# Kernel tuning notes

Hardware: AMD Instinct MI355X
Metric: run time of the kernel (lower is better)

Reference implementation:

```python
import jax, jax.numpy as jnp
import numpy as np

PS = 7        # pooled_size == conved_size
IMG = 300     # img_size
FMAP = 19     # feature map spatial size
SMAX = IMG // 16  # clamp max (18), matches torch long clamp(0, 300/16)
EPS = 1e-5


def _bn(x, g, b, m, v):
    scale = (g * jax.lax.rsqrt(v + EPS))[None, :, None, None]
    return x * scale + (b - m * g * jax.lax.rsqrt(v + EPS))[None, :, None, None]


def _conv(x, W, b=None, pad=1):
    y = jax.lax.conv_general_dilated(x, W, (1, 1), [(pad, pad), (pad, pad)],
                                     dimension_numbers=('NCHW', 'OIHW', 'NCHW'))
    if b is not None:
        y = y + b[None, :, None, None]
    return y


def _adaptive_w(lo, hi):
    # Per-ROI adaptive-avg-pool weights over the full 19-wide axis.
    # lo, hi: [B,R] inclusive crop bounds. Returns [B,R,PS,FMAP].
    H = hi - lo + 1                                  # crop length per ROI
    i = jnp.arange(PS)
    s = (i[None, None, :] * H[..., None]) // PS      # bin start (floor)
    e = -((-(i[None, None, :] + 1) * H[..., None]) // PS)  # bin end (ceil)
    rows = jnp.arange(FMAP)
    start = lo[..., None, None] + s[..., None]
    stop = lo[..., None, None] + e[..., None]
    mask = (rows >= start) & (rows < stop)
    denom = jnp.maximum(e - s, 1).astype(jnp.float32)[..., None]
    return mask.astype(jnp.float32) / denom


def setup_inputs() -> dict:
    key = jax.random.key(0)
    ks = jax.random.split(key, 6)
    B, R = 8, 128
    return {
        'roi_proposal': jax.random.uniform(ks[0], (B, 1, R, 5), dtype=jnp.float32),
        'features': jax.random.normal(ks[1], (B, 1024, FMAP, FMAP), dtype=jnp.float32),
        'W1': jax.random.normal(ks[2], (256, 1024, 3, 3), dtype=jnp.float32) * 0.02,
        'b1': jnp.zeros((256,), jnp.float32),
        'g1': jnp.ones((256,), jnp.float32),
        'be1': jnp.zeros((256,), jnp.float32),
        'm1': jnp.zeros((256,), jnp.float32),
        'v1': jnp.ones((256,), jnp.float32),
        'W2': jax.random.normal(ks[3], (256, 256, 3, 3), jnp.float32) * 0.05,
        'b2': jnp.zeros((256,), jnp.float32),
        'g2': jnp.ones((256,), jnp.float32),
        'be2': jnp.zeros((256,), jnp.float32),
        'm2': jnp.zeros((256,), jnp.float32),
        'v2': jnp.ones((256,), jnp.float32),
        'W3': jax.random.normal(ks[4], (32, 256, 1, 1), jnp.float32) * 0.1,
        'g3': jnp.ones((32,), jnp.float32),
        'be3': jnp.zeros((32,), jnp.float32),
        'm3': jnp.zeros((32,), jnp.float32),
        'v3': jnp.ones((32,), jnp.float32),
    }


def reference(roi_proposal, features, W1, b1, g1, be1, m1, v1,
              W2, b2, g2, be2, m2, v2, W3, g3, be3, m3, v3):
    # rois[..., 1:] * img_size / 16, then trunc to long (coords are >= 0)
    rl = (roi_proposal[:, 0, :, 1:] * (IMG / 16.0)).astype(jnp.int32)  # [B,R,4]
    c = jnp.clip(rl, 0, SMAX)
    xmin, ymin, xmax, ymax = c[..., 0], c[..., 1], c[..., 2], c[..., 3]
    valid = (xmax > xmin) & (ymax > ymin)                              # [B,R]
    B, R = valid.shape

    # fused crop + adaptive avg pool as two small pooling matmuls per ROI
    Wy = _adaptive_w(ymin, ymax)   # [B,R,7,19]
    Wx = _adaptive_w(xmin, xmax)   # [B,R,7,19]
    pooled = jnp.einsum('brph,bchw,brqw->brcpq', Wy, features, Wx)     # [B,R,1024,7,7]

    x = pooled.reshape(B * R, 1024, PS, PS)
    x = jax.nn.relu(_bn(_conv(x, W1, b1), g1, be1, m1, v1))
    x = jax.nn.relu(_bn(_conv(x, W2, b2), g2, be2, m2, v2))
    x = jax.nn.relu(_bn(_conv(x, W3, None, pad=0), g3, be3, m3, v3))
    out = x.reshape(B, R, 32, PS, PS) * valid[:, :, None, None, None]

    # compact valid ROIs to the front per batch (stable), invalid slots zeroed
    perm = jnp.argsort((~valid).astype(jnp.int32), axis=1, stable=True)
    out_c = jax.vmap(lambda o, p: o[p])(out, perm)                     # [B,R,32,7,7]
    er = rl.astype(jnp.float32) * (16.0 / IMG) * valid[..., None]
    er_c = jax.vmap(lambda o, p: o[p])(er, perm)[:, None]              # [B,1,R,4]
    keep_count = valid.sum(axis=1).astype(jnp.int32)                   # [B]
    return er_c, out_c, keep_count
```

## Files before the change

kernel.cpp:

```cpp
#include <hip/hip_runtime.h>
#include <cstddef>
#include <cstdint>

typedef unsigned short u16;
typedef unsigned int u32;
typedef __attribute__((ext_vector_type(8))) short short8;
typedef __attribute__((ext_vector_type(4))) float f32x4;

#define NB 8
#define NR 128
#define NPOS 49
#define EPSV 1e-5f
#define NSLOT 512

#define OUT_OC   4096
#define OUT_KEEP 1609728

static constexpr size_t OFF_META = 256;
static constexpr size_t OFF_KEEP = 33024;
static constexpr size_t OFF_W1Q  = 40960;
static constexpr size_t OFF_W2Q  = OFF_W1Q + 4718592;
static constexpr size_t OFF_W3   = OFF_W2Q + 1179648;
static constexpr size_t OFF_X1S  = OFF_W3  + 32768;
static constexpr size_t OFF_AP   = OFF_X1S + 13107200;
static constexpr size_t WS_NEED  = OFF_AP  + 51380224;

static __device__ __forceinline__ u16 f2bf(float f) {
  union { float f; u32 u; } x; x.f = f;
  u32 r = 0x7fffu + ((x.u >> 16) & 1u);
  return (u16)((x.u + r) >> 16);
}

__device__ __forceinline__ void int_body(const float* __restrict__ feat, float* __restrict__ S,
                                         int b, int cg, float* F)
{
  int tid = threadIdx.x;
  const float* fb = feat + ((size_t)b * 1024 + cg * 64) * 361;
#pragma unroll 1
  for (int i = tid; i < 64 * 361; i += 256) F[i] = fb[i];
  __syncthreads();
  if (tid < 64) {
    int ch = tid;
    const float* fp = F + ch * 361;
    float* Sp = S + (size_t)b * 400 * 1024 + cg * 64 + ch;
    float prev[20];
#pragma unroll
    for (int w = 0; w < 20; ++w) { prev[w] = 0.f; Sp[(size_t)w * 1024] = 0.f; }
    for (int h = 0; h < 19; ++h) {
      float run = 0.f;
      float* Sr = Sp + (size_t)(h + 1) * 20 * 1024;
      Sr[0] = 0.f;
#pragma unroll
      for (int w = 0; w < 19; ++w) {
        run += fp[h * 19 + w];
        float v = run + prev[w + 1];
        Sr[(size_t)(w + 1) * 1024] = v;
        prev[w + 1] = v;
      }
    }
  }
}

__device__ __forceinline__ void packw_body(const float* __restrict__ W, u16* __restrict__ wq,
                                           int IC, int c, int og, float* F)
{
  int tid = threadIdx.x, oc0 = og * 32;
#pragma unroll 1
  for (int i = tid; i < 18432; i += 256) {
    int ocr = i / 576, r = i - ocr * 576;
    F[i] = W[(size_t)(oc0 + ocr) * IC * 9 + c * 576 + r];
  }
  __syncthreads();
#pragma unroll 1
  for (int w = tid; w < 18432; w += 256) {
    int j = w & 7, lane = (w >> 3) & 63, rest = w >> 9;
    int ntr = rest & 1, kk = rest >> 1;
    int k9i = kk >> 1, ks = kk & 1;
    int ocr = ntr * 16 + (lane & 15);
    int icr = ks * 32 + ((lane >> 4) & 3) * 8 + j;
    int bid_ = (c * 9 + k9i) * 2 + ks;
    wq[((size_t)bid_ * 1024 + (oc0 / 16 + ntr) * 64 + lane) * 8 + j] = f2bf(F[ocr * 576 + icr * 9 + k9i]);
  }
}

__global__ __launch_bounds__(256) void k_prep(
    const float* __restrict__ feat, float* __restrict__ S,
    const float* __restrict__ W1, const float* __restrict__ W2, const float* __restrict__ W3,
    u16* __restrict__ w1q, u16* __restrict__ w2q, u16* __restrict__ w3q,
    const float* __restrict__ roi, int* __restrict__ cnt,
    int* __restrict__ meta, int* __restrict__ keepd, float* __restrict__ out)
{
  __shared__ float SH[23104];
  int bx = blockIdx.x;
  if (bx < 128) { int_body(feat, S, bx >> 4, bx & 15, SH); return; }
  if (bx < 256) { packw_body(W1, w1q, 1024, (bx - 128) >> 3, (bx - 128) & 7, SH); return; }
  if (bx < 288) { packw_body(W2, w2q, 256, (bx - 256) >> 3, (bx - 256) & 7, SH); return; }
  if (bx == 288) {
    for (int i = threadIdx.x; i < 8192; i += 256) {
      int oc = i >> 8, ic = i & 255;
      int kk = ic >> 5;
      int lane = ((ic >> 3) & 3) * 16 + (oc & 15);
      int nt16 = oc >> 4;
      int j = ic & 7;
      w3q[((size_t)((kk * 2 + nt16) * 64) + lane) * 8 + j] = f2bf(W3[i]);
    }
    return;
  }
  int b = bx - 289, t = threadIdx.x;
  int* sval = (int*)SH;
  int* spre = sval + 128;
  int rl[4], cl[4], valid = 0;
  if (t < 128) {
    const float* rp = roi + (size_t)(b * NR + t) * 5;
#pragma unroll
    for (int j = 0; j < 4; ++j) {
      rl[j] = (int)(rp[1 + j] * 18.75f);
      cl[j] = min(max(rl[j], 0), 18);
    }
    valid = (cl[2] > cl[0]) && (cl[3] > cl[1]) ? 1 : 0;
    sval[t] = valid;
  }
  __syncthreads();
  if (t == 0) {
    int s = 0;
    for (int i = 0; i < 128; ++i) { spre[i] = s; s += sval[i]; }
    spre[128] = s;
    keepd[b] = s;
    out[OUT_KEEP + b] = (float)s;
  }
  __syncthreads();
  if (t < 128) {
    int keep = spre[128];
    if (valid) {
      int dst = spre[t];
      int slot = atomicAdd(cnt, 1);
      int* mt = meta + slot * 8;
      mt[0] = b; mt[1] = dst;
      mt[2] = cl[1]; mt[3] = cl[3];
      mt[4] = cl[0]; mt[5] = cl[2];
#pragma unroll
      for (int j = 0; j < 4; ++j)
        out[(size_t)(b * NR + dst) * 4 + j] = (float)rl[j] * (16.0f / 300.0f);
    }
    if (t >= keep) {
#pragma unroll
      for (int j = 0; j < 4; ++j) out[(size_t)(b * NR + t) * 4 + j] = 0.f;
    }
  }
}

__global__ __launch_bounds__(256) void k_pool(
    const int* __restrict__ cnt, const int* __restrict__ meta,
    const float* __restrict__ S, u16* __restrict__ Apool)
{
  int cv = *cnt; if (cv > NSLOT) cv = NSLOT;
  int slot = blockIdx.x;
  if (slot >= cv) return;
  const int* mt_ = meta + slot * 8;
  int b = mt_[0], ylo = mt_[2], yhi = mt_[3], xlo = mt_[4], xhi = mt_[5];
  int Hy = yhi - ylo + 1, Hx = xhi - xlo + 1;
  const float* Sb = S + (size_t)b * 400 * 1024;
  u16* Ap = Apool + (size_t)slot * 50176;
  int base = blockIdx.y * 25088, end = base + 25088;
  int tid = threadIdx.x;
#pragma unroll 1
  for (int t0 = base + tid; t0 < end; t0 += 1024) {
#pragma unroll
    for (int u = 0; u < 4; ++u) {
      int t = t0 + u * 256;
      if (t < end) {
        int ch = t & 63, r = t >> 6;
        int bin = r % 49, c = r / 49;
        int p = bin / 7, q = bin - 7 * p;
        int sy = (p * Hy) / 7, ey = ((p + 1) * Hy + 6) / 7;
        int sx = (q * Hx) / 7, ex = ((q + 1) * Hx + 6) / 7;
        int y0 = ylo + sy, y1 = ylo + ey, x0 = xlo + sx, x1 = xlo + ex;
        const float* Sc = Sb + c * 64 + ch;
        float v = Sc[(size_t)(y1 * 20 + x1) * 1024] - Sc[(size_t)(y0 * 20 + x1) * 1024]
                - Sc[(size_t)(y1 * 20 + x0) * 1024] + Sc[(size_t)(y0 * 20 + x0) * 1024];
        v /= (float)((ey - sy) * (ex - sx));
        Ap[(size_t)c * 3136 + bin * 64 + ch] = f2bf(v);
      }
    }
  }
}

template<int STR>
__device__ __forceinline__ void build_aoffp(int n, int kq, int (&aoffp)[9][2]) {
#pragma unroll
  for (int t9 = 0; t9 < 9; ++t9) {
    int off[4];
#pragma unroll
    for (int mt = 0; mt < 4; ++mt) {
      int lm = mt * 16 + n;
      int mv = lm < 49;
      int lm2 = mv ? lm : 0;
      int p = lm2 / 7, q = lm2 - 7 * p;
      int ky = t9 / 3, kx = t9 - 3 * (t9 / 3);
      int ry = p + ky - 1, rx = q + kx - 1;
      int ok = mv && ry >= 0 && ry < 7 && rx >= 0 && rx < 7;
      int rr = ok ? ry * 7 + rx : 49;
      off[mt] = rr * STR + kq * 8;
    }
    aoffp[t9][0] = (off[0] & 0xFFFF) | (off[1] << 16);
    aoffp[t9][1] = (off[2] & 0xFFFF) | (off[3] << 16);
  }
}

__global__ __launch_bounds__(512) void k_conv1(
    const int* __restrict__ cnt, const u16* __restrict__ Apool, const u16* __restrict__ wq,
    const float* __restrict__ bb, const float* __restrict__ gg, const float* __restrict__ bec,
    const float* __restrict__ mm, const float* __restrict__ vv,
    u16* __restrict__ x1)
{
  int cv = *cnt; if (cv > NSLOT) cv = NSLOT;
  int slot0 = blockIdx.x * 4, ocq = blockIdx.y;
  if (slot0 >= cv) return;

  __shared__ __align__(16) u16 panels[16 * 3600];
  float* red = (float*)panels;

  int tid = threadIdx.x, lane = tid & 63, wave = tid >> 6;
  int kh = wave >> 2, roi4 = wave & 3;
  int n = lane & 15, kq = lane >> 4;

  for (int i = tid; i < 16 * 36; i += 512) {
    int sp = i / 36, w2 = i - sp * 36;
    ((u32*)(panels + sp * 3600 + 49 * 72))[w2] = 0;
  }

  int aoffp[9][2];
  build_aoffp<72>(n, kq, aoffp);
  f32x4 acc[4][4];
#pragma unroll
  for (int i = 0; i < 4; ++i)
#pragma unroll
    for (int j = 0; j < 4; ++j) acc[i][j] = (f32x4){0.f, 0.f, 0.f, 0.f};

  const u16* pf = wq + (size_t)(ocq * 4) * 512 + (size_t)lane * 8 + (size_t)(kh * 8) * 18 * 8192;
  short8 bbuf[2][4];
#pragma unroll
  for (int nt = 0; nt < 4; ++nt) bbuf[0][nt] = *(const short8*)(pf + nt * 512);
#pragma unroll
  for (int nt = 0; nt < 4; ++nt) bbuf[1][nt] = *(const short8*)(pf + 8192 + nt * 512);
  pf += (size_t)2 * 8192;

  uint4 sbuf[7];
  auto load_issue = [&](int ca, int cb) {
#pragma unroll
    for (int j = 0; j < 7; ++j) {
      int t = tid + j * 512;
      if (t < 3136) {
        int khs = t >= 1568 ? 1 : 0;
        int e2 = t - khs * 1568;
        int rr = e2 / 392, e = e2 - rr * 392;
        int c = khs ? cb : ca;
        int sl = slot0 + rr; if (sl >= cv) sl = cv - 1;
        sbuf[j] = *((const uint4*)(Apool + ((size_t)sl * 16 + c) * 3136) + e);
      }
    }
  };
  auto write_sbuf = [&](int B) {
#pragma unroll
    for (int j = 0; j < 7; ++j) {
      int t = tid + j * 512;
      if (t < 3136) {
        int khs = t >= 1568 ? 1 : 0;
        int e2 = t - khs * 1568;
        int rr = e2 / 392, e = e2 - rr * 392;
        *(uint4*)(panels + (size_t)((B * 2 + khs) * 4 + rr) * 3600 + (e >> 3) * 72 + (e & 7) * 8) = sbuf[j];
      }
    }
  };

  load_issue(0, 8);
  write_sbuf(0);
  __syncthreads();

#pragma unroll 1
  for (int i = 0; i < 8; ++i) {
    if (i + 1 < 8) load_issue(i + 1, 9 + i);
    const u16* P = panels + (size_t)(((i & 1) * 2 + kh) * 4 + roi4) * 3600;
#pragma unroll
    for (int kk = 0; kk < 18; ++kk) {
      int t9 = kk >> 1, ks = kk & 1;
      short8 bfr[4], afr[4];
#pragma unroll
      for (int nt = 0; nt < 4; ++nt) bfr[nt] = bbuf[kk & 1][nt];
#pragma unroll
      for (int nt = 0; nt < 4; ++nt) bbuf[kk & 1][nt] = *(const short8*)(pf + nt * 512);
      pf += 8192;
      int coff = ks * 32;
      int o0 = (aoffp[t9][0] & 0xFFFF) + coff, o1 = (int)((u32)aoffp[t9][0] >> 16) + coff;
      int o2 = (aoffp[t9][1] & 0xFFFF) + coff, o3 = (int)((u32)aoffp[t9][1] >> 16) + coff;
      afr[0] = *(const short8*)(P + o0); afr[1] = *(const short8*)(P + o1);
      afr[2] = *(const short8*)(P + o2); afr[3] = *(const short8*)(P + o3);
#pragma unroll
      for (int mt = 0; mt < 4; ++mt)
#pragma unroll
        for (int nt = 0; nt < 4; ++nt)
          acc[mt][nt] = __builtin_amdgcn_mfma_f32_16x16x32_bf16(afr[mt], bfr[nt], acc[mt][nt], 0, 0, 0);
    }
    if (i + 1 < 8) write_sbuf((i + 1) & 1);
    __syncthreads();
  }

  if (kh == 1) {
#pragma unroll
    for (int nt = 0; nt < 4; ++nt)
#pragma unroll
      for (int mt = 0; mt < 4; ++mt)
#pragma unroll
        for (int r = 0; r < 4; ++r) {
          int m = mt * 16 + kq * 4 + r;
          if (m < 49) red[((size_t)roi4 * 49 + m) * 64 + nt * 16 + n] = acc[mt][nt][r];
        }
  }
  __syncthreads();
  if (kh == 0) {
    int slot = slot0 + roi4;
    if (slot < cv) {
#pragma unroll
      for (int nt = 0; nt < 4; ++nt) {
        int oc = ocq * 64 + nt * 16 + n;
        float sc = gg[oc] * rsqrtf(vv[oc] + EPSV);
        float sh = (bb[oc] - mm[oc]) * sc + bec[oc];
#pragma unroll
        for (int mt = 0; mt < 4; ++mt)
#pragma unroll
          for (int r = 0; r < 4; ++r) {
            int m = mt * 16 + kq * 4 + r;
            if (m < 49) {
              float y = acc[mt][nt][r] + red[((size_t)roi4 * 49 + m) * 64 + nt * 16 + n];
              y = fmaf(y, sc, sh);
              x1[((size_t)slot * 4 + ocq) * 3136 + m * 64 + nt * 16 + n] = f2bf(y > 0.f ? y : 0.f);
            }
          }
      }
    }
  }
}

__global__ __launch_bounds__(512) void k_conv23(
    const int* __restrict__ cnt, const int* __restrict__ meta, const int* __restrict__ keepd,
    const u16* __restrict__ x1, const u16* __restrict__ w2q, const u16* __restrict__ w3q,
    const float* __restrict__ b2, const float* __restrict__ g2, const float* __restrict__ be2,
    const float* __restrict__ m2, const float* __restrict__ v2,
    const float* __restrict__ g3, const float* __restrict__ be3,
    const float* __restrict__ m3, const float* __restrict__ v3,
    float* __restrict__ out)
{
  int cv = *cnt; if (cv > NSLOT) cv = NSLOT;
  int slot = blockIdx.x;
  int tid = threadIdx.x;
  if (slot >= cv) {
    int nfill = NSLOT - cv;
#pragma unroll 1
    for (int j = slot - cv; j < 1024; j += nfill) {
      int b = j >> 7, dd = j & 127;
      if (dd >= keepd[b]) {
        float* o = out + OUT_OC + (size_t)(b * NR + dd) * 1568;
        for (int t = tid; t < 1568; t += 512) o[t] = 0.f;
      }
    }
    return;
  }
  const int* mt_ = meta + slot * 8;
  int b = mt_[0], dst = mt_[1];

  __shared__ __align__(16) char smem[77600];
  u16*   panels = (u16*)smem;
  float* red    = (float*)smem;
  u16*   xp     = (u16*)(smem + 51200);
  float* red3   = (float*)smem;

  int lane = tid & 63, wave = tid >> 6;
  int nt4 = wave & 3, kh = wave >> 2;
  int n = lane & 15, kq = lane >> 4;

  for (int i = tid; i < 4 * 36; i += 512) {
    int sp = i / 36, w2 = i - sp * 36;
    ((u32*)(panels + sp * 3600 + 49 * 72))[w2] = 0;
  }
  const u16* xs = x1 + (size_t)slot * 4 * 3136;
#pragma unroll 1
  for (int t = tid; t < 1568; t += 512) {
    int c = t / 392, e = t - c * 392;
    uint4 v = *((const uint4*)(xs + (size_t)c * 3136) + e);
    *(uint4*)(panels + (size_t)c * 3600 + (e >> 3) * 72 + (e & 7) * 8) = v;
  }

  int aoffp[9][2];
  build_aoffp<72>(n, kq, aoffp);
  f32x4 acc[4][4];
#pragma unroll
  for (int i = 0; i < 4; ++i)
#pragma unroll
    for (int j = 0; j < 4; ++j) acc[i][j] = (f32x4){0.f, 0.f, 0.f, 0.f};

  const u16* pf = w2q + (size_t)(nt4 * 4) * 512 + (size_t)lane * 8 + (size_t)(kh * 36) * 8192;
  short8 bbuf[3][4];
#pragma unroll
  for (int r2 = 0; r2 < 3; ++r2)
#pragma unroll
    for (int nt = 0; nt < 4; ++nt) bbuf[r2][nt] = *(const short8*)(pf + (size_t)r2 * 8192 + nt * 512);
  pf += (size_t)3 * 8192;

  __syncthreads();

#pragma unroll 1
  for (int ci = 0; ci < 2; ++ci) {
    const u16* P = panels + (size_t)(kh * 2 + ci) * 3600;
#pragma unroll
    for (int kk = 0; kk < 18; ++kk) {
      int t9 = kk >> 1, ks = kk & 1;
      short8 bfr[4], afr[4];
#pragma unroll
      for (int nt = 0; nt < 4; ++nt) bfr[nt] = bbuf[kk % 3][nt];
#pragma unroll
      for (int nt = 0; nt < 4; ++nt) bbuf[kk % 3][nt] = *(const short8*)(pf + nt * 512);
      pf += 8192;
      int coff = ks * 32;
      int o0 = (aoffp[t9][0] & 0xFFFF) + coff, o1 = (int)((u32)aoffp[t9][0] >> 16) + coff;
      int o2 = (aoffp[t9][1] & 0xFFFF) + coff, o3 = (int)((u32)aoffp[t9][1] >> 16) + coff;
      afr[0] = *(const short8*)(P + o0); afr[1] = *(const short8*)(P + o1);
      afr[2] = *(const short8*)(P + o2); afr[3] = *(const short8*)(P + o3);
#pragma unroll
      for (int mt = 0; mt < 4; ++mt)
#pragma unroll
        for (int nt = 0; nt < 4; ++nt)
          acc[mt][nt] = __builtin_amdgcn_mfma_f32_16x16x32_bf16(afr[mt], bfr[nt], acc[mt][nt], 0, 0, 0);
    }
  }
  __syncthreads();

  if (kh == 1) {
#pragma unroll
    for (int nt = 0; nt < 4; ++nt)
#pragma unroll
      for (int mt = 0; mt < 4; ++mt)
#pragma unroll
        for (int r = 0; r < 4; ++r) {
          int m = mt * 16 + kq * 4 + r;
          if (m < 49) red[((size_t)nt4 * 49 + m) * 64 + nt * 16 + n] = acc[mt][nt][r];
        }
  }
  __syncthreads();
  if (kh == 0) {
#pragma unroll
    for (int nt = 0; nt < 4; ++nt) {
      int oc = nt4 * 64 + nt * 16 + n;
      float sc = g2[oc] * rsqrtf(v2[oc] + EPSV);
      float sh = (b2[oc] - m2[oc]) * sc + be2[oc];
#pragma unroll
      for (int mt = 0; mt < 4; ++mt)
#pragma unroll
        for (int r = 0; r < 4; ++r) {
          int m = mt * 16 + kq * 4 + r;
          if (m < 49) {
            float y = acc[mt][nt][r] + red[((size_t)nt4 * 49 + m) * 64 + nt * 16 + n];
            y = fmaf(y, sc, sh);
            xp[m * 264 + oc] = f2bf(y > 0.f ? y : 0.f);
          }
        }
    }
  }
  if (wave == 4) {
    for (int i = lane; i < 132; i += 64) ((u32*)(xp + 49 * 264))[i] = 0;
  }
  __syncthreads();

  f32x4 a3[4][2];
#pragma unroll
  for (int mt = 0; mt < 4; ++mt) { a3[mt][0] = (f32x4){0,0,0,0}; a3[mt][1] = (f32x4){0,0,0,0}; }
  const u16* b3 = w3q + ((size_t)(wave * 2) * 64 + lane) * 8;
  short8 bf0 = *(const short8*)(b3);
  short8 bf1 = *(const short8*)(b3 + 512);
#pragma unroll
  for (int mt = 0; mt < 4; ++mt) {
    int m = mt * 16 + n;
    int row = m < 49 ? m : 49;
    short8 a = *(const short8*)(xp + row * 264 + wave * 32 + kq * 8);
    a3[mt][0] = __builtin_amdgcn_mfma_f32_16x16x32_bf16(a, bf0, a3[mt][0], 0, 0, 0);
    a3[mt][1] = __builtin_amdgcn_mfma_f32_16x16x32_bf16(a, bf1, a3[mt][1], 0, 0, 0);
  }
#pragma unroll
  for (int nt = 0; nt < 2; ++nt)
#pragma unroll
    for (int mt = 0; mt < 4; ++mt)
#pragma unroll
      for (int r = 0; r < 4; ++r) {
        int m = mt * 16 + kq * 4 + r;
        if (m < 49) red3[((size_t)wave * 49 + m) * 32 + nt * 16 + n] = a3[mt][nt][r];
      }
  __syncthreads();

  size_t ob = OUT_OC + ((size_t)(b * NR + dst) * 32) * 49;
#pragma unroll 1
  for (int t = tid; t < 1568; t += 512) {
    int m = t >> 5, oc = t & 31;
    float s = 0.f;
#pragma unroll
    for (int w8 = 0; w8 < 8; ++w8) s += red3[((size_t)w8 * 49 + m) * 32 + oc];
    float sc = g3[oc] * rsqrtf(v3[oc] + EPSV);
    float y = fmaf(s, sc, be3[oc] - m3[oc] * sc);
    out[ob + (size_t)oc * 49 + m] = y > 0.f ? y : 0.f;
  }
}

extern "C" void kernel_launch(void* const* d_in, const int* in_sizes, int n_in,
                              void* d_out, int out_size, void* d_ws, size_t ws_size,
                              hipStream_t stream)
{
  (void)in_sizes; (void)n_in; (void)out_size;
  if (ws_size < WS_NEED) return;

  const float* roi  = (const float*)d_in[0];
  const float* feat = (const float*)d_in[1];
  const float* W1   = (const float*)d_in[2];
  const float* b1   = (const float*)d_in[3];
  const float* g1   = (const float*)d_in[4];
  const float* be1  = (const float*)d_in[5];
  const float* m1   = (const float*)d_in[6];
  const float* v1   = (const float*)d_in[7];
  const float* W2   = (const float*)d_in[8];
  const float* b2   = (const float*)d_in[9];
  const float* g2   = (const float*)d_in[10];
  const float* be2  = (const float*)d_in[11];
  const float* m2   = (const float*)d_in[12];
  const float* v2   = (const float*)d_in[13];
  const float* W3   = (const float*)d_in[14];
  const float* g3   = (const float*)d_in[15];
  const float* be3  = (const float*)d_in[16];
  const float* m3   = (const float*)d_in[17];
  const float* v3   = (const float*)d_in[18];

  char* ws    = (char*)d_ws;
  int*  cnt   = (int*)ws;
  int*  meta  = (int*)(ws + OFF_META);
  int*  keepd = (int*)(ws + OFF_KEEP);
  u16*  w1q   = (u16*)(ws + OFF_W1Q);
  u16*  w2q   = (u16*)(ws + OFF_W2Q);
  u16*  w3q   = (u16*)(ws + OFF_W3);
  float* S    = (float*)(ws + OFF_X1S);
  u16*  x1    = (u16*)(ws + OFF_X1S);
  u16*  Apool = (u16*)(ws + OFF_AP);
  float* out  = (float*)d_out;

  hipMemsetAsync(cnt, 0, 4, stream);

  k_prep<<<297, 256, 0, stream>>>(feat, S, W1, W2, W3, w1q, w2q, w3q,
                                  roi, cnt, meta, keepd, out);
  k_pool<<<dim3(NSLOT, 2), 256, 0, stream>>>(cnt, meta, S, Apool);
  k_conv1<<<dim3(NSLOT / 4, 4), 512, 0, stream>>>(cnt, Apool, w1q, b1, g1, be1, m1, v1, x1);
  k_conv23<<<NSLOT, 512, 0, stream>>>(cnt, meta, keepd, x1, w2q, w3q,
                                      b2, g2, be2, m2, v2, g3, be3, m3, v3, out);
}
```

Before: 313.4 us.

## Single-buffer conv1 activation panels to raise occupancy

Drops the register-staged double buffer for the pooled activation panels in conv1. Each chunk is now loaded straight into a single LDS buffer between barriers, which halves shared memory and frees the 7 uint4 staging registers. The launch bound adds a minimum of 4 blocks per CU so more blocks can be resident at once. The cost is that global loads of the next chunk no longer overlap the MFMA loop, and each iteration gains an extra barrier, so the kernel now depends on occupancy to hide that load latency.

```diff
diff --git a/kernel.cpp b/kernel.cpp
--- a/kernel.cpp
+++ b/kernel.cpp
@@ -207,7 +207,7 @@
   }
 }
 
-__global__ __launch_bounds__(512) void k_conv1(
+__global__ __launch_bounds__(512, 4) void k_conv1(
     const int* __restrict__ cnt, const u16* __restrict__ Apool, const u16* __restrict__ wq,
     const float* __restrict__ bb, const float* __restrict__ gg, const float* __restrict__ bec,
     const float* __restrict__ mm, const float* __restrict__ vv,
@@ -217,14 +217,14 @@
   int slot0 = blockIdx.x * 4, ocq = blockIdx.y;
   if (slot0 >= cv) return;
 
-  __shared__ __align__(16) u16 panels[16 * 3600];
+  __shared__ __align__(16) u16 panels[8 * 3600];
   float* red = (float*)panels;
 
   int tid = threadIdx.x, lane = tid & 63, wave = tid >> 6;
   int kh = wave >> 2, roi4 = wave & 3;
   int n = lane & 15, kq = lane >> 4;
 
-  for (int i = tid; i < 16 * 36; i += 512) {
+  for (int i = tid; i < 8 * 36; i += 512) {
     int sp = i / 36, w2 = i - sp * 36;
     ((u32*)(panels + sp * 3600 + 49 * 72))[w2] = 0;
   }
@@ -245,42 +245,25 @@
   for (int nt = 0; nt < 4; ++nt) bbuf[1][nt] = *(const short8*)(pf + 8192 + nt * 512);
   pf += (size_t)2 * 8192;
 
-  uint4 sbuf[7];
-  auto load_issue = [&](int ca, int cb) {
-#pragma unroll
-    for (int j = 0; j < 7; ++j) {
-      int t = tid + j * 512;
-      if (t < 3136) {
-        int khs = t >= 1568 ? 1 : 0;
-        int e2 = t - khs * 1568;
-        int rr = e2 / 392, e = e2 - rr * 392;
-        int c = khs ? cb : ca;
-        int sl = slot0 + rr; if (sl >= cv) sl = cv - 1;
-        sbuf[j] = *((const uint4*)(Apool + ((size_t)sl * 16 + c) * 3136) + e);
-      }
+  auto stage = [&](int ca, int cb) {
+#pragma unroll 1
+    for (int t = tid; t < 3136; t += 512) {
+      int khs = t >= 1568 ? 1 : 0;
+      int e2 = t - khs * 1568;
+      int rr = e2 / 392, e = e2 - rr * 392;
+      int c = khs ? cb : ca;
+      int sl = slot0 + rr; if (sl >= cv) sl = cv - 1;
+      uint4 v = *((const uint4*)(Apool + ((size_t)sl * 16 + c) * 3136) + e);
+      *(uint4*)(panels + (size_t)(khs * 4 + rr) * 3600 + (e >> 3) * 72 + (e & 7) * 8) = v;
     }
   };
-  auto write_sbuf = [&](int B) {
-#pragma unroll
-    for (int j = 0; j < 7; ++j) {
-      int t = tid + j * 512;
-      if (t < 3136) {
-        int khs = t >= 1568 ? 1 : 0;
-        int e2 = t - khs * 1568;
-        int rr = e2 / 392, e = e2 - rr * 392;
-        *(uint4*)(panels + (size_t)((B * 2 + khs) * 4 + rr) * 3600 + (e >> 3) * 72 + (e & 7) * 8) = sbuf[j];
-      }
-    }
-  };
-
-  load_issue(0, 8);
-  write_sbuf(0);
-  __syncthreads();
-
+
+  stage(0, 8);
+  __syncthreads();
+
+  const u16* P = panels + (size_t)(kh * 4 + roi4) * 3600;
 #pragma unroll 1
   for (int i = 0; i < 8; ++i) {
-    if (i + 1 < 8) load_issue(i + 1, 9 + i);
-    const u16* P = panels + (size_t)(((i & 1) * 2 + kh) * 4 + roi4) * 3600;
 #pragma unroll
     for (int kk = 0; kk < 18; ++kk) {
       int t9 = kk >> 1, ks = kk & 1;
@@ -301,8 +284,11 @@
         for (int nt = 0; nt < 4; ++nt)
           acc[mt][nt] = __builtin_amdgcn_mfma_f32_16x16x32_bf16(afr[mt], bfr[nt], acc[mt][nt], 0, 0, 0);
     }
-    if (i + 1 < 8) write_sbuf((i + 1) & 1);
     __syncthreads();
+    if (i + 1 < 8) {
+      stage(i + 1, 9 + i);
+      __syncthreads();
+    }
   }
 
   if (kh == 1) {
```

New measurement: 333.6 us. 6.4% more time.
